# Performance work log

Hardware: AMD Instinct MI355X
Metric: run time of the kernel (lower is better)

Reference implementation:

```python
import jax, jax.numpy as jnp
import numpy as np
from jax import lax

HS, WS = 8, 8  # pattern_size


def setup_inputs() -> dict:
    key = jax.random.key(0)
    k1, k2, k3 = jax.random.split(key, 3)
    B, C, T, H, W = 2, 64, 16, 112, 112
    Cout, K = 64, 3
    x = jax.random.normal(k1, (B, C, T, H, W), dtype=jnp.float32)
    # one independent Conv3d weight/bias per (h, w) phase in the 8x8 pattern
    weight = jax.random.normal(k2, (HS, WS, Cout, C, K, K, K), dtype=jnp.float32) * 0.05
    bias = jax.random.normal(k3, (HS, WS, Cout), dtype=jnp.float32) * 0.05
    return {"x": x, "weight": weight, "bias": bias}


def reference(x, weight, bias):
    hs, ws = HS, WS
    B, C, T, H, W = x.shape
    Cout = weight.shape[2]
    # torch F.pad(x, (hs-1, hs-1, ws-1, ws-1, 1, 1)): W padded by hs-1, H by ws-1, T by 1
    paded = jnp.pad(x, ((0, 0), (0, 0), (1, 1), (ws - 1, ws - 1), (hs - 1, hs - 1)))
    Ho, Wo = H // hs, W // ws  # conv output spatial size per phase: (H-3)//8 + 1 = H//8
    rows = []
    for h in range(hs):
        cols = []
        for w in range(ws):
            sl = paded[:, :, :, h:H + h, w:W + w]  # [B, C, T+2, H, W]
            y = lax.conv_general_dilated(
                sl, weight[h, w],
                window_strides=(1, hs, ws), padding='VALID',
                dimension_numbers=('NCDHW', 'OIDHW', 'NCDHW'))  # [B, Cout, T, Ho, Wo]
            cols.append(y + bias[h, w][None, :, None, None, None])
        rows.append(jnp.stack(cols, 0))
    res = jnp.stack(rows, 0)  # [hs, ws, B, Cout, T, Ho, Wo]
    # out[:, :, :, h + hs*i, w + ws*j] = res[h, w, :, :, :, i, j]
    out = jnp.transpose(res, (2, 3, 4, 5, 0, 6, 1))  # [B, Cout, T, Ho, hs, Wo, ws]
    return out.reshape(B, Cout, T, H, W)
```

## Files before the change

### kernel.cpp

```cpp
#include <hip/hip_runtime.h>
#include <hip/hip_bf16.h>
#include <stdint.h>

typedef __attribute__((ext_vector_type(8))) short short8;
typedef __attribute__((ext_vector_type(4))) float f32x4;

#define XPP_BYTES 66355200ull
#define XPP_SLACK 65536ull
#define WPP_BYTES 14155776ull

__device__ __forceinline__ void gl2lds16(const void* g, void* l) {
    __builtin_amdgcn_global_load_lds(
        (const __attribute__((address_space(1))) unsigned int*)g,
        (__attribute__((address_space(3))) unsigned int*)l, 16, 0, 0);
}

__global__ __launch_bounds__(256)
void bzero(uint4* __restrict__ xpp) {
    const uint4 z = {0u, 0u, 0u, 0u};
    const int total = 935936;
    for (int idx = blockIdx.x * 256 + threadIdx.x; idx < total;
         idx += gridDim.x * 256) {
        int u;
        if (idx < 276480) {
            int slab = idx / 2160, off = idx % 2160;
            u = slab * 32400 + off;
        } else if (idx < 534528) {
            int k = idx - 276480;
            int run = k / 144, off = k % 144;
            int slab = run / 14, rho = run % 14 + 1;
            u = slab * 32400 + rho * 2160 + off;
        } else {
            int k = idx - 534528;
            int run = k / 8, off = k % 8;
            int slab = run / 392, r2 = run % 392;
            int rho = r2 / 28 + 1, r3 = r2 % 28;
            int cwo = r3 / 2 + 1, d = (r3 & 1) * 17;
            u = slab * 32400 + rho * 2160 + cwo * 144 + d * 8 + off;
        }
        xpp[u] = z;
    }
}

__global__ __launch_bounds__(512)
void xform_x(const float* __restrict__ xin, __hip_bfloat16* __restrict__ xpp) {
    extern __shared__ __hip_bfloat16 Xl[];
    const int bid = blockIdx.x;
    const int rho = bid % 14, d = (bid / 14) % 16, b = bid / 224;
    const int tid = threadIdx.x;
    for (int f = tid; f < 64 * 8 * 28; f += 512) {
        int ci = f / 224, rem = f % 224;
        int r = rem / 28, c4 = (rem % 28) * 4;
        const float4 v = *(const float4*)&xin[
            ((((size_t)b * 64 + ci) * 16 + d) * 112 + (rho * 8 + r)) * 112 + c4];
        const float vv[4] = {v.x, v.y, v.z, v.w};
#pragma unroll
        for (int u = 0; u < 4; ++u) {
            int c = c4 + u;
            Xl[(r * 112 + c) * 64 + (ci ^ ((c & 7) << 3))] = __float2bfloat16(vv[u]);
        }
    }
    __syncthreads();
    for (int f = tid; f < 896 * 8; f += 512) {
        int pos = f >> 3, j = f & 7;
        int r = pos / 112, c = pos % 112;
        int cw = c & 7, cwo = c >> 3;
        uint4 v = *(const uint4*)&Xl[pos * 64 + ((j * 8) ^ ((c & 7) << 3))];
        size_t dst = (((((size_t)(r * 8 + cw) * 2 + b) * 15 + (rho + 1)) * 15
                       + (cwo + 1)) * 18 + (d + 1)) * 64 + j * 8;
        *(uint4*)(xpp + dst) = v;
    }
}

__global__ __launch_bounds__(256)
void xform_w(const float* __restrict__ wt, __hip_bfloat16* __restrict__ wpp) {
    __shared__ __hip_bfloat16 lw[8 * 27 * 72];
    const int hw = blockIdx.x >> 3, cc = blockIdx.x & 7;
    for (int f = threadIdx.x; f < 8 * 64 * 27; f += 256) {
        int k = f % 27, ci = (f / 27) % 64, co = f / (27 * 64);
        float v = wt[(size_t)hw * 110592 + (size_t)(cc * 8 + co) * 1728 + ci * 27 + k];
        lw[(co * 27 + k) * 72 + ci] = __float2bfloat16(v);
    }
    __syncthreads();
    for (int f = threadIdx.x; f < 27 * 8 * 8; f += 256) {
        int cic = f % 8, co = (f / 8) % 8, k = f / 64;
        uint4 v = *(const uint4*)&lw[(co * 27 + k) * 72 + cic * 8];
        size_t dst = (((size_t)hw * 27 + k) * 64 + (cc * 8 + co)) * 64 + cic * 8;
        *(uint4*)(wpp + dst) = v;
    }
}

__global__ __launch_bounds__(256, 2)
void patgemm(const __hip_bfloat16* __restrict__ xpp,
             const __hip_bfloat16* __restrict__ wpp,
             const float* __restrict__ bs,
             float* __restrict__ out) {
    extern __shared__ char smem[];
    const int bid = blockIdx.x;
    const int h = bid & 7, k = bid >> 3;
    const int w = k & 7, b = (k >> 3) & 1, mc = k >> 4;
    const int hw = h * 8 + w;
    const int tid = threadIdx.x, wv = tid >> 6, lane = tid & 63;
    const int col = lane & 15, quad = lane >> 4;
    const int mg = wv >> 1, ng = wv & 1;

    uint32_t aoff[8];
#pragma unroll
    for (int i = 0; i < 8; ++i) {
        int slot = tid + i * 256;
        int wo = slot / 144, rem = slot % 144;
        int rt = rem >> 3, ch = rem & 7;
        aoff[i] = (uint32_t)(wo * 2304 + rt * 128 + ((ch ^ (rt & 7)) << 4));
    }
    uint32_t rofs[3][2];
#pragma unroll
    for (int kd = 0; kd < 3; ++kd)
#pragma unroll
        for (int ks = 0; ks < 2; ++ks)
            rofs[kd][ks] = (uint32_t)((col + kd) * 128
                + (((ks * 4 + quad) ^ ((col + kd) & 7)) << 4));
    const uint32_t bofs = (uint32_t)(col * 128 + quad * 16);

    f32x4 acc[7][2];
#pragma unroll
    for (int j = 0; j < 7; ++j)
#pragma unroll
        for (int n = 0; n < 2; ++n) acc[j][n] = (f32x4){0.f, 0.f, 0.f, 0.f};

    const char* wbase = (const char*)wpp + (size_t)hw * 27 * 8192;

    auto STAGE = [&](int bi, int rr) {
        const int kh = rr / 3, kw = rr % 3;
        const int r0 = h + kh - 7, c0 = w + kw - 7;
        const char* ap = (const char*)xpp +
            (size_t)(((((r0 & 7) * 8 + (c0 & 7)) * 2 + b) * 15
                      + ((r0 >> 3) + 1 + mc)) * 15 + ((c0 >> 3) + 1)) * 2304;
        char* Ad = smem + bi * 32768;
#pragma unroll
        for (int i = 0; i < 8; ++i)
            gl2lds16(ap + aoff[i], Ad + (uint32_t)(tid + i * 256) * 16);
    };

    STAGE(0, 0);
    __syncthreads();

#pragma unroll 1
    for (int rr = 0; rr < 9; ++rr) {
        const int cur = rr & 1;
        short8 bfr[12];
        const char* bp = wbase + (size_t)rr * 8192;
#pragma unroll
        for (int kd = 0; kd < 3; ++kd)
#pragma unroll
            for (int ks = 0; ks < 2; ++ks)
#pragma unroll
                for (int n = 0; n < 2; ++n)
                    bfr[kd * 4 + ks * 2 + n] = *(const short8*)(
                        bp + kd * 73728 + (ng * 2 + n) * 2048 + ks * 64 + bofs);
        __builtin_amdgcn_sched_barrier(0);
        if (rr < 8) STAGE(cur ^ 1, rr + 1);
        const char* Ab = smem + cur * 32768;
#pragma unroll
        for (int kd = 0; kd < 3; ++kd) {
#pragma unroll
            for (int ks = 0; ks < 2; ++ks) {
                short8 af[7];
#pragma unroll
                for (int j = 0; j < 7; ++j)
                    af[j] = *(const short8*)(Ab + (mg * 7 + j) * 2304 + rofs[kd][ks]);
                __builtin_amdgcn_s_setprio(1);
#pragma unroll
                for (int j = 0; j < 7; ++j)
#pragma unroll
                    for (int n = 0; n < 2; ++n)
                        acc[j][n] = __builtin_amdgcn_mfma_f32_16x16x32_bf16(
                            af[j], bfr[kd * 4 + ks * 2 + n], acc[j][n], 0, 0, 0);
                __builtin_amdgcn_s_setprio(0);
            }
        }
        __syncthreads();
    }

    const float* bsl = bs + hw * 64;
    const int y = 8 * mc + h;
#pragma unroll
    for (int j = 0; j < 7; ++j) {
        const int wo = mg * 7 + j;
        const int x = 8 * wo + w;
#pragma unroll
        for (int n = 0; n < 2; ++n) {
            const int co = (ng * 2 + n) * 16 + col;
            const float bv = bsl[co];
#pragma unroll
            for (int jj = 0; jj < 4; ++jj) {
                const int t = quad * 4 + jj;
                out[((((size_t)b * 64 + co) * 16 + t) * 112 + y) * 112 + x]
                    = acc[j][n][jj] + bv;
            }
        }
    }
}

#define XL_ROWSTRIDE 116
#define WL_WSTRIDE (17*27)

__global__ __launch_bounds__(256, 3)
void patconv3d_fp32(const float* __restrict__ xin,
                    const float* __restrict__ wt,
                    const float* __restrict__ bs,
                    float* __restrict__ out) {
    __shared__ float Xl[3*3*7*XL_ROWSTRIDE];
    __shared__ float Wl[8*WL_WSTRIDE];
    const int bid = blockIdx.x;
    const int ct = bid & 3, hb = (bid >> 2) & 1, h = (bid >> 3) & 7;
    const int t = (bid >> 6) & 15, b = (bid >> 10) & 1;
    const int tid = threadIdx.x;
    const int xl = tid & 127, cg = tid >> 7;
    const int xr = (xl < 112) ? xl : 111;
    const int wq = xl & 7;
    float acc[8][7];
#pragma unroll
    for (int c = 0; c < 8; ++c)
#pragma unroll
        for (int ho = 0; ho < 7; ++ho) acc[c][ho] = 0.f;
    for (int ci = 0; ci < 64; ++ci) {
        __syncthreads();
        for (int idx = tid; idx < 3 * 3 * 7 * 114; idx += 256) {
            int c = idx % 114, rest = idx / 114;
            int ho = rest % 7; rest /= 7;
            int kh = rest % 3, kd = rest / 3;
            int r = 8 * (hb * 7 + ho) + h + kh - 7;
            int d = t + kd - 1, colx = c - 7;
            float v = 0.f;
            if (r >= 0 && d >= 0 && d < 16 && colx >= 0)
                v = xin[(((size_t)(b * 64 + ci) * 16 + d) * 112 + r) * 112 + colx];
            Xl[((kd * 3 + kh) * 7 + ho) * XL_ROWSTRIDE + c] = v;
        }
        for (int idx = tid; idx < 8 * 16 * 27; idx += 256) {
            int k = idx % 27, rest = idx / 27;
            int co_l = rest % 16, wi = rest / 16;
            Wl[wi * WL_WSTRIDE + co_l * 27 + k] =
                wt[(((size_t)(h * 8 + wi) * 64 + (ct * 16 + co_l)) * 64 + ci) * 27 + k];
        }
        __syncthreads();
#pragma unroll
        for (int kd = 0; kd < 3; ++kd)
#pragma unroll
            for (int kh = 0; kh < 3; ++kh)
#pragma unroll
                for (int kw = 0; kw < 3; ++kw) {
                    const int k = (kd * 3 + kh) * 3 + kw;
                    float xv[7];
#pragma unroll
                    for (int ho = 0; ho < 7; ++ho)
                        xv[ho] = Xl[((kd * 3 + kh) * 7 + ho) * XL_ROWSTRIDE + xr + kw];
                    float wv[8];
#pragma unroll
                    for (int c = 0; c < 8; ++c)
                        wv[c] = Wl[wq * WL_WSTRIDE + (cg * 8 + c) * 27 + k];
#pragma unroll
                    for (int c = 0; c < 8; ++c)
#pragma unroll
                        for (int ho = 0; ho < 7; ++ho)
                            acc[c][ho] += wv[c] * xv[ho];
                }
    }
    if (xl < 112) {
#pragma unroll
        for (int c = 0; c < 8; ++c) {
            const int co = ct * 16 + cg * 8 + c;
            const float bv = bs[(h * 8 + wq) * 64 + co];
#pragma unroll
            for (int ho = 0; ho < 7; ++ho) {
                const int y = 8 * (hb * 7 + ho) + h;
                out[(((size_t)(b * 64 + co) * 16 + t) * 112 + y) * 112 + xl] = acc[c][ho] + bv;
            }
        }
    }
}

extern "C" void kernel_launch(void* const* d_in, const int* in_sizes, int n_in,
                              void* d_out, int out_size, void* d_ws, size_t ws_size,
                              hipStream_t stream) {
    const float* x  = (const float*)d_in[0];
    const float* wg = (const float*)d_in[1];
    const float* bi = (const float*)d_in[2];
    float* out = (float*)d_out;
    if (ws_size >= XPP_BYTES + XPP_SLACK + WPP_BYTES) {
        __hip_bfloat16* xpp = (__hip_bfloat16*)d_ws;
        __hip_bfloat16* wpp = (__hip_bfloat16*)((char*)d_ws + XPP_BYTES + XPP_SLACK);
        bzero<<<1024, 256, 0, stream>>>((uint4*)d_ws);
        xform_x<<<448, 512, 114688, stream>>>(x, xpp);
        xform_w<<<512, 256, 0, stream>>>(wg, wpp);
        patgemm<<<1792, 256, 65536, stream>>>(xpp, wpp, bi, out);
    } else {
        patconv3d_fp32<<<2048, 256, 0, stream>>>(x, wg, bi, out);
    }
}
```

Before: 294.9 us.

## Split A staging into half-K chunks with 4-deep LDS ring and B double-buffering

Result: slower. 303.0 us (+2.7%).

```diff
diff --git a/kernel.cpp b/kernel.cpp
--- a/kernel.cpp
+++ b/kernel.cpp
@@ -90,6 +90,65 @@
     }
 }
 
+
+#define STG(S) do {                                                          \
+    const int s3_ = (S);                                                     \
+    const int rr_ = s3_ >> 1, kh_ = rr_ / 3, kw_ = rr_ % 3;                  \
+    const int r0_ = h + kh_ - 7, c0_ = w + kw_ - 7;                          \
+    const char* ap_ = (const char*)xpp +                                     \
+        (size_t)(((((r0_ & 7) * 8 + (c0_ & 7)) * 2 + b) * 15                 \
+                  + ((r0_ >> 3) + 1 + mc)) * 15 + ((c0_ >> 3) + 1)) * 2304   \
+        + (s3_ & 1) * 64;                                                    \
+    char* Ad_ = smem + (s3_ & 3) * 16384;                                    \
+    _Pragma("unroll")                                                        \
+    for (int i_ = 0; i_ < 4; ++i_)                                           \
+        gl2lds16(ap_ + srcoff[i_], Ad_ + (uint32_t)(tid + i_ * 256) * 16);   \
+} while (0)
+
+#define LDB(R, DST) do {                                                     \
+    const char* bp_ = wbase + (size_t)(R) * 8192;                            \
+    _Pragma("unroll")                                                        \
+    for (int kd_ = 0; kd_ < 3; ++kd_)                                        \
+    _Pragma("unroll")                                                        \
+    for (int ks_ = 0; ks_ < 2; ++ks_)                                        \
+    _Pragma("unroll")                                                        \
+    for (int n_ = 0; n_ < 2; ++n_)                                           \
+        DST[kd_ * 4 + ks_ * 2 + n_] = *(const short8*)(                      \
+            bp_ + kd_ * 73728 + (ng * 2 + n_) * 2048 + ks_ * 64 + bofs);     \
+} while (0)
+
+#define WINDOW(S, R, CUR, NXT, KS, DOB, DOA, WAITN) do {                     \
+    if ((WAITN) == 0)      asm volatile("s_waitcnt vmcnt(0)" ::: "memory");  \
+    else if ((WAITN) == 4) asm volatile("s_waitcnt vmcnt(4)" ::: "memory");  \
+    else if ((WAITN) == 8) asm volatile("s_waitcnt vmcnt(8)" ::: "memory");  \
+    else                   asm volatile("s_waitcnt vmcnt(20)" ::: "memory"); \
+    __builtin_amdgcn_s_barrier();                                            \
+    {   const char* Ab_ = smem + ((S) & 3) * 16384;                          \
+        _Pragma("unroll")                                                    \
+        for (int kd = 0; kd < 3; ++kd) {                                     \
+            short8 af_[7];                                                   \
+            _Pragma("unroll")                                                \
+            for (int j_ = 0; j_ < 7; ++j_)                                   \
+                af_[j_] = *(const short8*)(Ab_ + (mg * 7 + j_) * 1152        \
+                                           + rofs[kd]);                      \
+            if (kd == 0) {                                                   \
+                __builtin_amdgcn_sched_barrier(0);                           \
+                if (DOB) LDB((R) + 1, NXT);                                  \
+                if (DOA) STG((S) + 3);                                       \
+                __builtin_amdgcn_sched_barrier(0);                           \
+            }                                                                \
+            __builtin_amdgcn_s_setprio(1);                                   \
+            _Pragma("unroll")                                                \
+            for (int j_ = 0; j_ < 7; ++j_)                                   \
+                _Pragma("unroll")                                            \
+                for (int n_ = 0; n_ < 2; ++n_)                               \
+                    acc[j_][n_] = __builtin_amdgcn_mfma_f32_16x16x32_bf16(   \
+                        af_[j_], CUR[kd * 4 + (KS) * 2 + n_],                \
+                        acc[j_][n_], 0, 0, 0);                               \
+            __builtin_amdgcn_s_setprio(0);                                   \
+        } }                                                                  \
+} while (0)
+
 __global__ __launch_bounds__(256, 2)
 void patgemm(const __hip_bfloat16* __restrict__ xpp,
              const __hip_bfloat16* __restrict__ wpp,
@@ -104,21 +163,19 @@
     const int col = lane & 15, quad = lane >> 4;
     const int mg = wv >> 1, ng = wv & 1;
 
-    uint32_t aoff[8];
-#pragma unroll
-    for (int i = 0; i < 8; ++i) {
-        int slot = tid + i * 256;
-        int wo = slot / 144, rem = slot % 144;
-        int rt = rem >> 3, ch = rem & 7;
-        aoff[i] = (uint32_t)(wo * 2304 + rt * 128 + ((ch ^ (rt & 7)) << 4));
-    }
-    uint32_t rofs[3][2];
+    uint32_t srcoff[4];
+#pragma unroll
+    for (int i = 0; i < 4; ++i) {
+        int u = tid + i * 256; if (u > 1007) u = 1007;
+        int wo = u / 72, rem = u % 72;
+        int d = rem >> 2, qp = rem & 3, q = qp ^ ((d >> 1) & 3);
+        srcoff[i] = (uint32_t)(wo * 2304 + d * 128 + q * 16);
+    }
+    uint32_t rofs[3];
 #pragma unroll
     for (int kd = 0; kd < 3; ++kd)
-#pragma unroll
-        for (int ks = 0; ks < 2; ++ks)
-            rofs[kd][ks] = (uint32_t)((col + kd) * 128
-                + (((ks * 4 + quad) ^ ((col + kd) & 7)) << 4));
+        rofs[kd] = (uint32_t)((col + kd) * 64
+            + ((quad ^ (((col + kd) >> 1) & 3)) << 4));
     const uint32_t bofs = (uint32_t)(col * 128 + quad * 16);
 
     f32x4 acc[7][2];
@@ -128,58 +185,25 @@
         for (int n = 0; n < 2; ++n) acc[j][n] = (f32x4){0.f, 0.f, 0.f, 0.f};
 
     const char* wbase = (const char*)wpp + (size_t)hw * 27 * 8192;
-
-    auto STAGE = [&](int bi, int rr) {
-        const int kh = rr / 3, kw = rr % 3;
-        const int r0 = h + kh - 7, c0 = w + kw - 7;
-        const char* ap = (const char*)xpp +
-            (size_t)(((((r0 & 7) * 8 + (c0 & 7)) * 2 + b) * 15
-                      + ((r0 >> 3) + 1 + mc)) * 15 + ((c0 >> 3) + 1)) * 2304;
-        char* Ad = smem + bi * 32768;
-#pragma unroll
-        for (int i = 0; i < 8; ++i)
-            gl2lds16(ap + aoff[i], Ad + (uint32_t)(tid + i * 256) * 16);
-    };
-
-    STAGE(0, 0);
-    __syncthreads();
+    short8 bfrA[12], bfrB[12];
+
+    STG(0);
+    __builtin_amdgcn_sched_barrier(0);
+    LDB(0, bfrA);
+    __builtin_amdgcn_sched_barrier(0);
+    STG(1);
+    STG(2);
 
 #pragma unroll 1
-    for (int rr = 0; rr < 9; ++rr) {
-        const int cur = rr & 1;
-        short8 bfr[12];
-        const char* bp = wbase + (size_t)rr * 8192;
-#pragma unroll
-        for (int kd = 0; kd < 3; ++kd)
-#pragma unroll
-            for (int ks = 0; ks < 2; ++ks)
-#pragma unroll
-                for (int n = 0; n < 2; ++n)
-                    bfr[kd * 4 + ks * 2 + n] = *(const short8*)(
-                        bp + kd * 73728 + (ng * 2 + n) * 2048 + ks * 64 + bofs);
-        __builtin_amdgcn_sched_barrier(0);
-        if (rr < 8) STAGE(cur ^ 1, rr + 1);
-        const char* Ab = smem + cur * 32768;
-#pragma unroll
-        for (int kd = 0; kd < 3; ++kd) {
-#pragma unroll
-            for (int ks = 0; ks < 2; ++ks) {
-                short8 af[7];
-#pragma unroll
-                for (int j = 0; j < 7; ++j)
-                    af[j] = *(const short8*)(Ab + (mg * 7 + j) * 2304 + rofs[kd][ks]);
-                __builtin_amdgcn_s_setprio(1);
-#pragma unroll
-                for (int j = 0; j < 7; ++j)
-#pragma unroll
-                    for (int n = 0; n < 2; ++n)
-                        acc[j][n] = __builtin_amdgcn_mfma_f32_16x16x32_bf16(
-                            af[j], bfr[kd * 4 + ks * 2 + n], acc[j][n], 0, 0, 0);
-                __builtin_amdgcn_s_setprio(0);
-            }
-        }
-        __syncthreads();
-    }
+    for (int rp = 0; rp < 4; ++rp) {
+        const int ra = 2 * rp, rb = 2 * rp + 1;
+        WINDOW(2 * ra,     ra, bfrA, bfrB, 0, 1, 1, 8);
+        WINDOW(2 * ra + 1, ra, bfrA, bfrB, 1, 0, 1, 20);
+        WINDOW(2 * rb,     rb, bfrB, bfrA, 0, 1, 1, 8);
+        WINDOW(2 * rb + 1, rb, bfrB, bfrA, 1, 0, (rb < 7), 20);
+    }
+    WINDOW(16, 8, bfrA, bfrB, 0, 0, 0, 4);
+    WINDOW(17, 8, bfrA, bfrB, 1, 0, 0, 0);
 
     const float* bsl = bs + hw * 64;
     const int y = 8 * mc + h;
@@ -237,10 +261,10 @@
             Xl[((kd * 3 + kh) * 7 + ho) * XL_ROWSTRIDE + c] = v;
         }
         for (int idx = tid; idx < 8 * 16 * 27; idx += 256) {
-            int k = idx % 27, rest = idx / 27;
+            int k2 = idx % 27, rest = idx / 27;
             int co_l = rest % 16, wi = rest / 16;
-            Wl[wi * WL_WSTRIDE + co_l * 27 + k] =
-                wt[(((size_t)(h * 8 + wi) * 64 + (ct * 16 + co_l)) * 64 + ci) * 27 + k];
+            Wl[wi * WL_WSTRIDE + co_l * 27 + k2] =
+                wt[(((size_t)(h * 8 + wi) * 64 + (ct * 16 + co_l)) * 64 + ci) * 27 + k2];
         }
         __syncthreads();
 #pragma unroll
@@ -249,7 +273,7 @@
             for (int kh = 0; kh < 3; ++kh)
 #pragma unroll
                 for (int kw = 0; kw < 3; ++kw) {
-                    const int k = (kd * 3 + kh) * 3 + kw;
+                    const int k2 = (kd * 3 + kh) * 3 + kw;
                     float xv[7];
 #pragma unroll
                     for (int ho = 0; ho < 7; ++ho)
@@ -257,7 +281,7 @@
                     float wv[8];
 #pragma unroll
                     for (int c = 0; c < 8; ++c)
-                        wv[c] = Wl[wq * WL_WSTRIDE + (cg * 8 + c) * 27 + k];
+                        wv[c] = Wl[wq * WL_WSTRIDE + (cg * 8 + c) * 27 + k2];
 #pragma unroll
                     for (int c = 0; c < 8; ++c)
 #pragma unroll
```

## Stage weights through LDS and split A tile into half-K double-buffered stages

Applied to the files above, without the earlier changes.

Result: faster. 255.8 us, median of 2 (-13.2%).

```diff
diff --git a/kernel.cpp b/kernel.cpp
--- a/kernel.cpp
+++ b/kernel.cpp
@@ -5,9 +5,8 @@
 typedef __attribute__((ext_vector_type(8))) short short8;
 typedef __attribute__((ext_vector_type(4))) float f32x4;
 
+#define WPP_BYTES 14155776ull
 #define XPP_BYTES 66355200ull
-#define XPP_SLACK 65536ull
-#define WPP_BYTES 14155776ull
 
 __device__ __forceinline__ void gl2lds16(const void* g, void* l) {
     __builtin_amdgcn_global_load_lds(
@@ -90,36 +89,45 @@
     }
 }
 
+
 __global__ __launch_bounds__(256, 2)
 void patgemm(const __hip_bfloat16* __restrict__ xpp,
-             const __hip_bfloat16* __restrict__ wpp,
+             const char* __restrict__ wppc,
              const float* __restrict__ bs,
              float* __restrict__ out) {
     extern __shared__ char smem[];
+    const char* xppc = (const char*)xpp;
     const int bid = blockIdx.x;
-    const int h = bid & 7, k = bid >> 3;
-    const int w = k & 7, b = (k >> 3) & 1, mc = k >> 4;
+    const int h = bid & 7, w = (bid >> 3) & 7, b = (bid >> 6) & 1, mc = bid >> 7;
     const int hw = h * 8 + w;
-    const int tid = threadIdx.x, wv = tid >> 6, lane = tid & 63;
-    const int col = lane & 15, quad = lane >> 4;
+    const int tid = threadIdx.x, wv = tid >> 6;
+    const int lane = tid & 63, col = lane & 15, quad = lane >> 4;
     const int mg = wv >> 1, ng = wv & 1;
 
-    uint32_t aoff[8];
-#pragma unroll
-    for (int i = 0; i < 8; ++i) {
-        int slot = tid + i * 256;
-        int wo = slot / 144, rem = slot % 144;
-        int rt = rem >> 3, ch = rem & 7;
-        aoff[i] = (uint32_t)(wo * 2304 + rt * 128 + ((ch ^ (rt & 7)) << 4));
-    }
-    uint32_t rofs[3][2];
-#pragma unroll
-    for (int kd = 0; kd < 3; ++kd)
-#pragma unroll
-        for (int ks = 0; ks < 2; ++ks)
-            rofs[kd][ks] = (uint32_t)((col + kd) * 128
-                + (((ks * 4 + quad) ^ ((col + kd) & 7)) << 4));
-    const uint32_t bofs = (uint32_t)(col * 128 + quad * 16);
+    uint32_t aoff[4];
+#pragma unroll
+    for (int i = 0; i < 4; ++i) {
+        int u = tid + i * 256; if (u > 1007) u = 1007;
+        int wo = u / 72, rem = u - wo * 72;
+        int d = rem >> 2, qp = rem & 3, q = qp ^ ((d >> 1) & 3);
+        aoff[i] = (uint32_t)(wo * 2304 + d * 128 + q * 16);
+    }
+    uint32_t boff[2];
+#pragma unroll
+    for (int i = 0; i < 2; ++i) {
+        int u = tid + i * 256;
+        boff[i] = (uint32_t)((u >> 3) * 128 + (((u & 7) ^ ((u >> 3) & 7)) << 4));
+    }
+    uint32_t rofs[3];
+#pragma unroll
+    for (int kd = 0; kd < 3; ++kd) {
+        int d = col + kd;
+        rofs[kd] = (uint32_t)(d * 64 + ((quad ^ ((d >> 1) & 3)) << 4));
+    }
+    uint32_t bofsw[2];
+#pragma unroll
+    for (int hf = 0; hf < 2; ++hf)
+        bofsw[hf] = (uint32_t)(col * 128 + (((hf * 4 + quad) ^ (col & 7)) << 4));
 
     f32x4 acc[7][2];
 #pragma unroll
@@ -127,55 +135,65 @@
 #pragma unroll
         for (int n = 0; n < 2; ++n) acc[j][n] = (f32x4){0.f, 0.f, 0.f, 0.f};
 
-    const char* wbase = (const char*)wpp + (size_t)hw * 27 * 8192;
-
-    auto STAGE = [&](int bi, int rr) {
-        const int kh = rr / 3, kw = rr % 3;
+    const char* wbase = wppc + (size_t)hw * 221184;
+
+    auto lineBase = [&](int p) -> const char* {
+        const int kh = (p >= 6) ? 2 : (p >= 3 ? 1 : 0);
+        const int kw = p - 3 * kh;
         const int r0 = h + kh - 7, c0 = w + kw - 7;
-        const char* ap = (const char*)xpp +
-            (size_t)(((((r0 & 7) * 8 + (c0 & 7)) * 2 + b) * 15
-                      + ((r0 >> 3) + 1 + mc)) * 15 + ((c0 >> 3) + 1)) * 2304;
-        char* Ad = smem + bi * 32768;
-#pragma unroll
-        for (int i = 0; i < 8; ++i)
-            gl2lds16(ap + aoff[i], Ad + (uint32_t)(tid + i * 256) * 16);
+        return xppc + (size_t)(((((r0 & 7) * 8 + (c0 & 7)) * 2 + b) * 15
+                    + ((r0 >> 3) + 1 + mc)) * 15 + ((c0 >> 3) + 1)) * 2304;
     };
-
-    STAGE(0, 0);
+    auto STGA = [&](const char* lb, int hf, int buf) {
+#pragma unroll
+        for (int i = 0; i < 4; ++i)
+            gl2lds16(lb + aoff[i] + hf * 64,
+                     smem + buf * 16384 + (tid + i * 256) * 16);
+    };
+    auto STGB = [&](int tap, int slot) {
+#pragma unroll
+        for (int i = 0; i < 2; ++i)
+            gl2lds16(wbase + (size_t)tap * 8192 + boff[i],
+                     smem + 32768 + slot * 8192 + (tid + i * 256) * 16);
+    };
+
+    const char* lb = lineBase(0);
+    STGA(lb, 0, 0);
+    STGB(0, 0); STGB(9, 1); STGB(18, 2);
     __syncthreads();
 
 #pragma unroll 1
-    for (int rr = 0; rr < 9; ++rr) {
-        const int cur = rr & 1;
-        short8 bfr[12];
-        const char* bp = wbase + (size_t)rr * 8192;
-#pragma unroll
-        for (int kd = 0; kd < 3; ++kd)
-#pragma unroll
-            for (int ks = 0; ks < 2; ++ks)
-#pragma unroll
-                for (int n = 0; n < 2; ++n)
-                    bfr[kd * 4 + ks * 2 + n] = *(const short8*)(
-                        bp + kd * 73728 + (ng * 2 + n) * 2048 + ks * 64 + bofs);
-        __builtin_amdgcn_sched_barrier(0);
-        if (rr < 8) STAGE(cur ^ 1, rr + 1);
-        const char* Ab = smem + cur * 32768;
+    for (int p = 0; p < 9; ++p) {
+        const int pp = p & 1;
+        STGA(lb, 1, 1);
+        if (p < 8) {
+            const int sb = (1 - pp) * 3;
+            STGB(p + 1, sb); STGB(p + 10, sb + 1); STGB(p + 19, sb + 2);
+        }
 #pragma unroll
         for (int kd = 0; kd < 3; ++kd) {
-#pragma unroll
-            for (int ks = 0; ks < 2; ++ks) {
-                short8 af[7];
-#pragma unroll
-                for (int j = 0; j < 7; ++j)
-                    af[j] = *(const short8*)(Ab + (mg * 7 + j) * 2304 + rofs[kd][ks]);
-                __builtin_amdgcn_s_setprio(1);
-#pragma unroll
-                for (int j = 0; j < 7; ++j)
-#pragma unroll
-                    for (int n = 0; n < 2; ++n)
-                        acc[j][n] = __builtin_amdgcn_mfma_f32_16x16x32_bf16(
-                            af[j], bfr[kd * 4 + ks * 2 + n], acc[j][n], 0, 0, 0);
-                __builtin_amdgcn_s_setprio(0);
+            const char* Bb = smem + 32768 + (pp * 3 + kd) * 8192;
+            short8 bf0 = *(const short8*)(Bb + (ng * 2 + 0) * 2048 + bofsw[0]);
+            short8 bf1 = *(const short8*)(Bb + (ng * 2 + 1) * 2048 + bofsw[0]);
+#pragma unroll
+            for (int j = 0; j < 7; ++j) {
+                short8 af = *(const short8*)(smem + (mg * 7 + j) * 1152 + rofs[kd]);
+                acc[j][0] = __builtin_amdgcn_mfma_f32_16x16x32_bf16(af, bf0, acc[j][0], 0, 0, 0);
+                acc[j][1] = __builtin_amdgcn_mfma_f32_16x16x32_bf16(af, bf1, acc[j][1], 0, 0, 0);
+            }
+        }
+        __syncthreads();
+        if (p < 8) { lb = lineBase(p + 1); STGA(lb, 0, 0); }
+#pragma unroll
+        for (int kd = 0; kd < 3; ++kd) {
+            const char* Bb = smem + 32768 + (pp * 3 + kd) * 8192;
+            short8 bf0 = *(const short8*)(Bb + (ng * 2 + 0) * 2048 + bofsw[1]);
+            short8 bf1 = *(const short8*)(Bb + (ng * 2 + 1) * 2048 + bofsw[1]);
+#pragma unroll
+            for (int j = 0; j < 7; ++j) {
+                short8 af = *(const short8*)(smem + 16384 + (mg * 7 + j) * 1152 + rofs[kd]);
+                acc[j][0] = __builtin_amdgcn_mfma_f32_16x16x32_bf16(af, bf0, acc[j][0], 0, 0, 0);
+                acc[j][1] = __builtin_amdgcn_mfma_f32_16x16x32_bf16(af, bf1, acc[j][1], 0, 0, 0);
             }
         }
         __syncthreads();
@@ -185,8 +203,7 @@
     const int y = 8 * mc + h;
 #pragma unroll
     for (int j = 0; j < 7; ++j) {
-        const int wo = mg * 7 + j;
-        const int x = 8 * wo + w;
+        const int x = 8 * (mg * 7 + j) + w;
 #pragma unroll
         for (int n = 0; n < 2; ++n) {
             const int co = (ng * 2 + n) * 16 + col;
@@ -237,10 +254,10 @@
             Xl[((kd * 3 + kh) * 7 + ho) * XL_ROWSTRIDE + c] = v;
         }
         for (int idx = tid; idx < 8 * 16 * 27; idx += 256) {
-            int k = idx % 27, rest = idx / 27;
+            int k2 = idx % 27, rest = idx / 27;
             int co_l = rest % 16, wi = rest / 16;
-            Wl[wi * WL_WSTRIDE + co_l * 27 + k] =
-                wt[(((size_t)(h * 8 + wi) * 64 + (ct * 16 + co_l)) * 64 + ci) * 27 + k];
+            Wl[wi * WL_WSTRIDE + co_l * 27 + k2] =
+                wt[(((size_t)(h * 8 + wi) * 64 + (ct * 16 + co_l)) * 64 + ci) * 27 + k2];
         }
         __syncthreads();
 #pragma unroll
@@ -249,7 +266,7 @@
             for (int kh = 0; kh < 3; ++kh)
 #pragma unroll
                 for (int kw = 0; kw < 3; ++kw) {
-                    const int k = (kd * 3 + kh) * 3 + kw;
+                    const int k2 = (kd * 3 + kh) * 3 + kw;
                     float xv[7];
 #pragma unroll
                     for (int ho = 0; ho < 7; ++ho)
@@ -257,7 +274,7 @@
                     float wv[8];
 #pragma unroll
                     for (int c = 0; c < 8; ++c)
-                        wv[c] = Wl[wq * WL_WSTRIDE + (cg * 8 + c) * 27 + k];
+                        wv[c] = Wl[wq * WL_WSTRIDE + (cg * 8 + c) * 27 + k2];
 #pragma unroll
                     for (int c = 0; c < 8; ++c)
 #pragma unroll
@@ -286,13 +303,13 @@
     const float* wg = (const float*)d_in[1];
     const float* bi = (const float*)d_in[2];
     float* out = (float*)d_out;
-    if (ws_size >= XPP_BYTES + XPP_SLACK + WPP_BYTES) {
-        __hip_bfloat16* xpp = (__hip_bfloat16*)d_ws;
-        __hip_bfloat16* wpp = (__hip_bfloat16*)((char*)d_ws + XPP_BYTES + XPP_SLACK);
-        bzero<<<1024, 256, 0, stream>>>((uint4*)d_ws);
+    if (ws_size >= WPP_BYTES + XPP_BYTES) {
+        __hip_bfloat16* wpp = (__hip_bfloat16*)d_ws;
+        __hip_bfloat16* xpp = (__hip_bfloat16*)((char*)d_ws + WPP_BYTES);
+        bzero<<<1024, 256, 0, stream>>>((uint4*)xpp);
         xform_x<<<448, 512, 114688, stream>>>(x, xpp);
         xform_w<<<512, 256, 0, stream>>>(wg, wpp);
-        patgemm<<<1792, 256, 65536, stream>>>(xpp, wpp, bi, out);
+        patgemm<<<1792, 256, 81920, stream>>>(xpp, (const char*)wpp, bi, out);
     } else {
         patconv3d_fp32<<<2048, 256, 0, stream>>>(x, wg, bi, out);
     }
```
